# Kernel optimization log

Hardware: AMD Instinct MI355X
Metric: run time of the kernel (lower is better)

Reference implementation:

```python
import jax, jax.numpy as jnp
import numpy as np

NUM_HEADS = 8

def setup_inputs() -> dict:
    key = jax.random.key(0)
    k1, k2, k3 = jax.random.split(key, 3)
    query = jax.random.normal(k1, (2, 2048, 512), jnp.float32)   # [B, Tq, out_DIM]
    value = jax.random.normal(k2, (2, 2048, 64), jnp.float32)    # [B, Tv, out_DIM//H]
    conv_w = jax.random.normal(k3, (512, 64, 1), jnp.float32) * 0.05  # Conv1d weight [out, in, 1]
    conv_b = jnp.zeros((512,), jnp.float32)
    return {"query": query, "value": value, "conv_w": conv_w, "conv_b": conv_b}

def reference(query, value, conv_w, conv_b):
    B, Tq, D = query.shape
    H = NUM_HEADS
    dh = D // H  # 64
    # Conv1d with kernel_size=1 over the feature axis == pointwise linear
    k = jnp.einsum('btd,od->bto', value, conv_w[:, :, 0]) + conv_b  # [B, Tv, D]
    Tv = k.shape[1]
    # split heads
    qs = query.reshape(B, Tq, H, dh).transpose(0, 2, 1, 3)  # [B,H,Tq,dh]
    ks = k.reshape(B, Tv, H, dh).transpose(0, 2, 1, 3)      # [B,H,Tv,dh]
    vs = jnp.broadcast_to(value[:, None], (B, H, Tv, dh))   # v repeated per head
    # scaled dot product (normalize=True)
    qk = jnp.einsum('bhqd,bhkd->bhqk', qs, ks) * (dh ** -0.5)  # [B,H,Tq,Tv]
    # F.softmax(qk) with no dim on a 4D tensor uses legacy implicit dim=1 (heads)
    weights = jax.nn.softmax(qk, axis=1)
    ctx = jnp.einsum('bhqk,bhkd->bhqd', weights, vs)  # [B,H,Tq,dh]
    # combine heads
    return ctx.transpose(0, 2, 1, 3).reshape(B, Tq, H * dh)  # [B,Tq,D]
```

## Files before the change

kernel.cpp:

```cpp
#include <hip/hip_runtime.h>
#include <hip/hip_bf16.h>

#define BATCH 2
#define TSEQ  2048
#define DMODEL 512
#define NHEAD 8
#define DHEAD 64

typedef __bf16 bf16x2 __attribute__((ext_vector_type(2)));
typedef __bf16 bf16x4 __attribute__((ext_vector_type(4)));
typedef __bf16 bf16x8 __attribute__((ext_vector_type(8)));
typedef float  f32x4  __attribute__((ext_vector_type(4)));

#if __has_builtin(__builtin_amdgcn_exp2f)
#define EXP2(x) __builtin_amdgcn_exp2f(x)
#else
#define EXP2(x) exp2f(x)
#endif

__device__ __forceinline__ bf16x8 load_b8(const void* p) {
  return __builtin_bit_cast(bf16x8, *reinterpret_cast<const uint4*>(p));
}

__device__ __forceinline__ bf16x8 cvt8(const float* p) {
  float4 a = *reinterpret_cast<const float4*>(p);
  float4 b = *reinterpret_cast<const float4*>(p + 4);
  bf16x8 r;
  r[0] = (__bf16)a.x; r[1] = (__bf16)a.y; r[2] = (__bf16)a.z; r[3] = (__bf16)a.w;
  r[4] = (__bf16)b.x; r[5] = (__bf16)b.y; r[6] = (__bf16)b.z; r[7] = (__bf16)b.w;
  return r;
}

__device__ __forceinline__ bf16x8 cvt8s(const float* p, float s) {
  float4 a = *reinterpret_cast<const float4*>(p);
  float4 b = *reinterpret_cast<const float4*>(p + 4);
  bf16x8 r;
  r[0] = (__bf16)(a.x * s); r[1] = (__bf16)(a.y * s);
  r[2] = (__bf16)(a.z * s); r[3] = (__bf16)(a.w * s);
  r[4] = (__bf16)(b.x * s); r[5] = (__bf16)(b.y * s);
  r[6] = (__bf16)(b.z * s); r[7] = (__bf16)(b.w * s);
  return r;
}

__device__ __forceinline__ uint packbf(float a, float b) {
  uint ua = __builtin_bit_cast(uint, a);
  uint ub = __builtin_bit_cast(uint, b);
  return (ua >> 16) | (ub & 0xFFFF0000u);
}

#define KT_B   1048576
#define KT_T   8192
#define VT_B   131072
#define VT_K   2048

__global__ __launch_bounds__(256) void conv_kernel(
    const float* __restrict__ V,
    const float* __restrict__ W,
    const float* __restrict__ bias,
    __hip_bfloat16* __restrict__ Kt) {
  const int bx = blockIdx.x;
  const int b    = bx >> 7;
  const int tset = bx & 127;
  const int t0   = tset << 4;
  const int w  = threadIdx.x >> 6;
  const int l  = threadIdx.x & 63;
  const int lm = l & 15;
  const int lg = l >> 4;

  const float* vrow = V + ((size_t)(b * TSEQ + t0 + lm)) * DHEAD;
  bf16x8 av0 = cvt8(vrow + lg * 8);
  bf16x8 av1 = cvt8(vrow + 32 + lg * 8);

  #pragma unroll
  for (int n = 0; n < 8; ++n) {
    const int o0 = (w * 8 + n) * 16;
    const float* wrow = W + ((size_t)(o0 + lm)) * DHEAD;
    bf16x8 b0 = cvt8(wrow + lg * 8);
    bf16x8 b1 = cvt8(wrow + 32 + lg * 8);
    f32x4 acc = {0.f, 0.f, 0.f, 0.f};
    acc = __builtin_amdgcn_mfma_f32_16x16x32_bf16(av0, b0, acc, 0, 0, 0);
    acc = __builtin_amdgcn_mfma_f32_16x16x32_bf16(av1, b1, acc, 0, 0, 0);
    const int o   = o0 + lm;
    const int h   = o >> 6;
    const int gg  = (o >> 5) & 1;
    const int lgt = (o >> 3) & 3;
    const int j   = o & 7;
    const float bv = bias[o];
    const size_t kbase = (size_t)b * KT_B + (size_t)tset * KT_T +
                         h * 1024 + gg * 512 + lgt * 128 + j;
    #pragma unroll
    for (int r = 0; r < 4; ++r)
      Kt[kbase + (size_t)(lg * 4 + r) * 8] = __float2bfloat16(acc[r] + bv);
  }
}

__global__ __launch_bounds__(256) void vt_kernel(const float* __restrict__ V,
                                                 __hip_bfloat16* __restrict__ Vtile) {
  const int bx = blockIdx.x;
  const int b  = bx >> 5;
  const int t0 = (bx & 31) << 6;
  const int tid = threadIdx.x;
  __shared__ float tile[64][65];

  #pragma unroll
  for (int p = 0; p < 4; ++p) {
    const int r = p * 16 + (tid >> 4);
    const int c = (tid & 15) * 4;
    float4 v = *reinterpret_cast<const float4*>(
        &V[((size_t)(b * TSEQ + t0 + r)) * DHEAD + c]);
    tile[r][c]     = v.x;
    tile[r][c + 1] = v.y;
    tile[r][c + 2] = v.z;
    tile[r][c + 3] = v.w;
  }
  __syncthreads();

  const int dt = tid >> 6;
  const int l  = tid & 63;
  const int lm = l & 15;
  const int lg = l >> 4;
  #pragma unroll
  for (int ks2 = 0; ks2 < 2; ++ks2) {
    bf16x8 o;
    #pragma unroll
    for (int jj = 0; jj < 4; ++jj) {
      o[jj]     = (__bf16)tile[ks2 * 32 + lg * 4 + jj][dt * 16 + lm];
      o[jj + 4] = (__bf16)tile[ks2 * 32 + 16 + lg * 4 + jj][dt * 16 + lm];
    }
    *reinterpret_cast<uint4*>(
        Vtile + (size_t)b * VT_B + (size_t)((t0 >> 5) + ks2) * VT_K +
        dt * 512 + l * 8) = __builtin_bit_cast(uint4, o);
  }
}

template <int KCH>
__global__ __launch_bounds__(256, 2) void attn_kernel(
    const float* __restrict__ Q,
    const __hip_bfloat16* __restrict__ Kt,
    const __hip_bfloat16* __restrict__ Vtile,
    float* __restrict__ Out,
    float* __restrict__ P) {
  const int bx = blockIdx.x;
  int b, q0, c;
  if (KCH == 2) {
    const int L = (bx & 7) * 64 + (bx >> 3);
    b = L >> 8; const int rest = L & 255; q0 = (rest >> 1) << 4; c = rest & 1;
  } else {
    const int L = (bx & 7) * 32 + (bx >> 3);
    b = L >> 7; q0 = (L & 127) << 4; c = 0;
  }
  const int tid = threadIdx.x;
  const int w  = tid >> 6;
  const int l  = tid & 63;
  const int lm = l & 15;
  const int lg = l >> 4;

  constexpr int NRND = KCH == 2 ? 8 : 16;
  const int tsbase = c * 64;
  const int kvbase = c * 32;

  __shared__ __bf16 Qs[16 * 512];
  __shared__ __bf16 Ws[4][NHEAD][512];
  __shared__ float  Obuf[64][17];

  const float cl2 = 0.125f * 1.44269504f;
  {
    const int row = tid >> 4;
    const int seg = tid & 15;
    const float* src = Q + ((size_t)(b * TSEQ + q0 + row)) * DMODEL + seg * 32;
    char* base = (char*)Qs;
    const int sw = (row & 7) << 4;
    #pragma unroll
    for (int u = 0; u < 4; ++u) {
      bf16x8 v = cvt8s(src + u * 8, cl2);
      *(bf16x8*)(base + ((row * 1024 + seg * 64 + u * 16) ^ sw)) = v;
    }
  }
  __syncthreads();

  f32x4 accO[NHEAD];
  #pragma unroll
  for (int h = 0; h < NHEAD; ++h) accO[h] = (f32x4){0.f, 0.f, 0.f, 0.f};

  const char* qb = (const char*)Qs;
  const int qsw = (lm & 7) << 4;

  bf16x8 vA[4], vB[4];

  #define S_HALF(TSET, S2)                                                    \
    {                                                                         \
      const __hip_bfloat16* kb_ =                                             \
          Kt + (size_t)b * KT_B + (size_t)(TSET) * KT_T + l * 8;              \
      bf16x8 kf0[NHEAD], kf1[NHEAD];                                          \
      _Pragma("unroll")                                                       \
      for (int h = 0; h < NHEAD; ++h) {                                       \
        kf0[h] = load_b8(kb_ + h * 1024);                                     \
        kf1[h] = load_b8(kb_ + h * 1024 + 512);                               \
      }                                                                       \
      f32x4 sv[NHEAD];                                                        \
      __builtin_amdgcn_s_setprio(1);                                          \
      _Pragma("unroll")                                                       \
      for (int h = 0; h < NHEAD; ++h) {                                       \
        bf16x8 q0_ = *(const bf16x8*)(qb + ((lm * 1024 + h * 128 + lg * 16) ^ qsw)); \
        bf16x8 q1_ = *(const bf16x8*)(qb + ((lm * 1024 + h * 128 + 64 + lg * 16) ^ qsw)); \
        f32x4 t = {0.f, 0.f, 0.f, 0.f};                                       \
        t = __builtin_amdgcn_mfma_f32_16x16x32_bf16(kf0[h], q0_, t, 0, 0, 0); \
        t = __builtin_amdgcn_mfma_f32_16x16x32_bf16(kf1[h], q1_, t, 0, 0, 0); \
        sv[h] = t;                                                            \
      }                                                                       \
      __builtin_amdgcn_s_setprio(0);                                          \
      _Pragma("unroll")                                                       \
      for (int rp = 0; rp < 2; ++rp) {                                        \
        float w0_[NHEAD], w1_[NHEAD];                                         \
        float s0_ = 0.f, s1_ = 0.f;                                           \
        _Pragma("unroll")                                                     \
        for (int h = 0; h < NHEAD; ++h) { w0_[h] = EXP2(sv[h][2 * rp]);     s0_ += w0_[h]; } \
        _Pragma("unroll")                                                     \
        for (int h = 0; h < NHEAD; ++h) { w1_[h] = EXP2(sv[h][2 * rp + 1]); s1_ += w1_[h]; } \
        const float i0_ = __builtin_amdgcn_rcpf(s0_);                         \
        const float i1_ = __builtin_amdgcn_rcpf(s1_);                         \
        _Pragma("unroll")                                                     \
        for (int h = 0; h < NHEAD; ++h)                                       \
          wfu[h][(S2) * 2 + rp] = packbf(w0_[h] * i0_, w1_[h] * i1_);         \
      }                                                                       \
    }

  #define ROUND(R, VCUR, VNXT)                                                \
    {                                                                         \
      uint wfu[NHEAD][4];                                                     \
      const int ts0 = tsbase + (R) * 8 + w * 2;                               \
      S_HALF(ts0, 0);                                                         \
      S_HALF(ts0 + 1, 1);                                                     \
      _Pragma("unroll")                                                       \
      for (int h = 0; h < NHEAD; ++h)                                         \
        *reinterpret_cast<uint4*>((char*)(&Ws[w][h][0]) + l * 16) =           \
            uint4{wfu[h][0], wfu[h][1], wfu[h][2], wfu[h][3]};                \
      {                                                                       \
        const int RN = (R) < NRND - 1 ? (R) + 1 : NRND - 1;                   \
        const __hip_bfloat16* vb_ = Vtile + (size_t)b * VT_B +                \
            (size_t)(kvbase + RN * 4) * VT_K + w * 512 + l * 8;               \
        _Pragma("unroll")                                                     \
        for (int s = 0; s < 4; ++s) VNXT[s] = load_b8(vb_ + s * 2048);        \
      }                                                                       \
      __syncthreads();                                                        \
      __builtin_amdgcn_s_setprio(1);                                          \
      _Pragma("unroll")                                                       \
      for (int s = 0; s < 4; ++s) {                                           \
        _Pragma("unroll")                                                     \
        for (int h = 0; h < NHEAD; ++h) {                                     \
          bf16x8 wsf = *(const bf16x8*)((const char*)(&Ws[s][h][0]) + l * 16);\
          accO[h] = __builtin_amdgcn_mfma_f32_16x16x32_bf16(VCUR[s], wsf, accO[h], 0, 0, 0); \
        }                                                                     \
      }                                                                       \
      __builtin_amdgcn_s_setprio(0);                                          \
      __syncthreads();                                                        \
    }

  {
    const __hip_bfloat16* vb_ = Vtile + (size_t)b * VT_B +
        (size_t)kvbase * VT_K + w * 512 + l * 8;
    #pragma unroll
    for (int s = 0; s < 4; ++s) vA[s] = load_b8(vb_ + s * 2048);
  }

  #pragma unroll 1
  for (int rp2 = 0; rp2 < NRND / 2; ++rp2) {
    ROUND(2 * rp2,     vA, vB);
    ROUND(2 * rp2 + 1, vB, vA);
  }

  #undef ROUND
  #undef S_HALF

  float* outbase = (KCH == 2)
      ? P + ((size_t)((b * 128 + (q0 >> 4)) * 2 + c)) * 8192
      : Out + ((size_t)(b * TSEQ + q0)) * DMODEL;
  #pragma unroll
  for (int h = 0; h < NHEAD; ++h) {
    #pragma unroll
    for (int r = 0; r < 4; ++r)
      Obuf[w * 16 + lg * 4 + r][lm] = accO[h][r];
    __syncthreads();
    {
      const int q  = tid >> 4;
      const int d0 = (tid & 15) * 4;
      float4 s = {Obuf[d0][q], Obuf[d0 + 1][q], Obuf[d0 + 2][q], Obuf[d0 + 3][q]};
      *reinterpret_cast<float4*>(&outbase[(size_t)q * 512 + h * DHEAD + d0]) = s;
    }
    __syncthreads();
  }
}

__global__ void reduce_kernel(const float4* __restrict__ P,
                              float4* __restrict__ Out) {
  const int g = blockIdx.x * 256 + threadIdx.x;
  const int f = g << 2;
  const int d = f & 511;
  const int q = (f >> 9) & 2047;
  const int b = f >> 20;
  const size_t p0 = (((size_t)(b * 128 + (q >> 4)) * 2) * 8192 +
                     (size_t)(q & 15) * 512 + d) >> 2;
  float4 a = P[p0];
  float4 c = P[p0 + 2048];
  Out[g] = float4{a.x + c.x, a.y + c.y, a.z + c.z, a.w + c.w};
}

extern "C" void kernel_launch(void* const* d_in, const int* in_sizes, int n_in,
                              void* d_out, int out_size, void* d_ws, size_t ws_size,
                              hipStream_t stream) {
  const float* Q    = (const float*)d_in[0];
  const float* V    = (const float*)d_in[1];
  const float* W    = (const float*)d_in[2];
  const float* bias = (const float*)d_in[3];
  float* Out = (float*)d_out;

  __hip_bfloat16* Ktb = (__hip_bfloat16*)d_ws;
  __hip_bfloat16* Vtb = Ktb + (size_t)BATCH * KT_B;
  const size_t pOff = 4u * 1024 * 1024 + 512u * 1024;
  float* P = (float*)((char*)d_ws + pOff);
  const bool split = ws_size >= pOff + (size_t)512 * 8192 * 4;

  conv_kernel<<<256, 256, 0, stream>>>(V, W, bias, Ktb);
  vt_kernel<<<64, 256, 0, stream>>>(V, Vtb);
  if (split) {
    attn_kernel<2><<<512, 256, 0, stream>>>(Q, Ktb, Vtb, Out, P);
    reduce_kernel<<<2048, 256, 0, stream>>>((const float4*)P, (float4*)Out);
  } else {
    attn_kernel<1><<<256, 256, 0, stream>>>(Q, Ktb, Vtb, Out, P);
  }
}
```

Measured before the change: 53.88 us.

## Replace split-KV attention plus reduce with single 512-thread block per query tile

Drops the two-chunk KV split and its separate reduction kernel, launching 256 blocks of 512 threads (8 waves) that each cover the full key range for a 16-query tile. Each wave computes scores for 2 key tiles per round, and in the PV step each wave handles 4 heads by one 16-column d-slice. The Q shared-memory layout is changed to a per-head linear layout without swizzle, and V prefetch double-buffering is replaced by a per-round load of 8 fragments. This removes the partial-sum write, the reduce launch and its memory traffic. In exchange it uses fewer, larger blocks with one block per CU, and it loses the V prefetch overlap.

After: 71.98 us. 33.6% more time.

```diff
diff --git a/kernel.cpp b/kernel.cpp
--- a/kernel.cpp
+++ b/kernel.cpp
@@ -133,79 +133,64 @@
   }
 }
 
-template <int KCH>
-__global__ __launch_bounds__(256, 2) void attn_kernel(
+__global__ __launch_bounds__(512, 1) void attn_kernel(
     const float* __restrict__ Q,
     const __hip_bfloat16* __restrict__ Kt,
     const __hip_bfloat16* __restrict__ Vtile,
-    float* __restrict__ Out,
-    float* __restrict__ P) {
+    float* __restrict__ Out) {
   const int bx = blockIdx.x;
-  int b, q0, c;
-  if (KCH == 2) {
-    const int L = (bx & 7) * 64 + (bx >> 3);
-    b = L >> 8; const int rest = L & 255; q0 = (rest >> 1) << 4; c = rest & 1;
-  } else {
-    const int L = (bx & 7) * 32 + (bx >> 3);
-    b = L >> 7; q0 = (L & 127) << 4; c = 0;
-  }
+  const int L  = (bx & 7) * 32 + (bx >> 3);
+  const int b  = L >> 7;
+  const int q0 = (L & 127) << 4;
   const int tid = threadIdx.x;
-  const int w  = tid >> 6;
-  const int l  = tid & 63;
-  const int lm = l & 15;
-  const int lg = l >> 4;
-
-  constexpr int NRND = KCH == 2 ? 8 : 16;
-  const int tsbase = c * 64;
-  const int kvbase = c * 32;
-
-  __shared__ __bf16 Qs[16 * 512];
-  __shared__ __bf16 Ws[4][NHEAD][512];
-  __shared__ float  Obuf[64][17];
+  const int w   = tid >> 6;
+  const int l   = tid & 63;
+  const int lm  = l & 15;
+  const int lg  = l >> 4;
+  const int myh0 = (w >> 2) * 4;
+  const int mydt = w & 3;
+
+  __shared__ __bf16 Qs[8192];
+  __shared__ __bf16 Ws[8][NHEAD][512];
+  __shared__ float  Obuf[2][64][17];
 
   const float cl2 = 0.125f * 1.44269504f;
   {
-    const int row = tid >> 4;
-    const int seg = tid & 15;
-    const float* src = Q + ((size_t)(b * TSEQ + q0 + row)) * DMODEL + seg * 32;
-    char* base = (char*)Qs;
-    const int sw = (row & 7) << 4;
-    #pragma unroll
-    for (int u = 0; u < 4; ++u) {
-      bf16x8 v = cvt8s(src + u * 8, cl2);
-      *(bf16x8*)(base + ((row * 1024 + seg * 64 + u * 16) ^ sw)) = v;
+    const int hg = tid >> 5;
+    const int wi = tid & 31;
+    const int h = hg >> 1, g = hg & 1;
+    #pragma unroll
+    for (int u = 0; u < 2; ++u) {
+      const int ll  = u * 32 + wi;
+      const int row = ll & 15;
+      const int seg = ll >> 4;
+      const float* src = Q + ((size_t)(b * TSEQ + q0 + row)) * DMODEL +
+                         h * DHEAD + g * 32 + seg * 8;
+      bf16x8 v = cvt8s(src, cl2);
+      *(bf16x8*)((char*)Qs + hg * 1024 + ll * 16) = v;
     }
   }
   __syncthreads();
 
-  f32x4 accO[NHEAD];
-  #pragma unroll
-  for (int h = 0; h < NHEAD; ++h) accO[h] = (f32x4){0.f, 0.f, 0.f, 0.f};
-
-  const char* qb = (const char*)Qs;
-  const int qsw = (lm & 7) << 4;
-
-  bf16x8 vA[4], vB[4];
+  f32x4 accO[4];
+  #pragma unroll
+  for (int hh = 0; hh < 4; ++hh) accO[hh] = (f32x4){0.f, 0.f, 0.f, 0.f};
 
   #define S_HALF(TSET, S2)                                                    \
     {                                                                         \
       const __hip_bfloat16* kb_ =                                             \
           Kt + (size_t)b * KT_B + (size_t)(TSET) * KT_T + l * 8;              \
-      bf16x8 kf0[NHEAD], kf1[NHEAD];                                          \
-      _Pragma("unroll")                                                       \
-      for (int h = 0; h < NHEAD; ++h) {                                       \
-        kf0[h] = load_b8(kb_ + h * 1024);                                     \
-        kf1[h] = load_b8(kb_ + h * 1024 + 512);                               \
-      }                                                                       \
       f32x4 sv[NHEAD];                                                        \
       __builtin_amdgcn_s_setprio(1);                                          \
       _Pragma("unroll")                                                       \
       for (int h = 0; h < NHEAD; ++h) {                                       \
-        bf16x8 q0_ = *(const bf16x8*)(qb + ((lm * 1024 + h * 128 + lg * 16) ^ qsw)); \
-        bf16x8 q1_ = *(const bf16x8*)(qb + ((lm * 1024 + h * 128 + 64 + lg * 16) ^ qsw)); \
+        bf16x8 kf0 = load_b8(kb_ + h * 1024);                                 \
+        bf16x8 kf1 = load_b8(kb_ + h * 1024 + 512);                           \
+        bf16x8 q0_ = *(const bf16x8*)((const char*)Qs + (h * 2) * 1024 + l * 16);     \
+        bf16x8 q1_ = *(const bf16x8*)((const char*)Qs + (h * 2 + 1) * 1024 + l * 16); \
         f32x4 t = {0.f, 0.f, 0.f, 0.f};                                       \
-        t = __builtin_amdgcn_mfma_f32_16x16x32_bf16(kf0[h], q0_, t, 0, 0, 0); \
-        t = __builtin_amdgcn_mfma_f32_16x16x32_bf16(kf1[h], q1_, t, 0, 0, 0); \
+        t = __builtin_amdgcn_mfma_f32_16x16x32_bf16(kf0, q0_, t, 0, 0, 0);    \
+        t = __builtin_amdgcn_mfma_f32_16x16x32_bf16(kf1, q1_, t, 0, 0, 0);    \
         sv[h] = t;                                                            \
       }                                                                       \
       __builtin_amdgcn_s_setprio(0);                                          \
@@ -225,84 +210,60 @@
       }                                                                       \
     }
 
-  #define ROUND(R, VCUR, VNXT)                                                \
-    {                                                                         \
-      uint wfu[NHEAD][4];                                                     \
-      const int ts0 = tsbase + (R) * 8 + w * 2;                               \
-      S_HALF(ts0, 0);                                                         \
-      S_HALF(ts0 + 1, 1);                                                     \
-      _Pragma("unroll")                                                       \
-      for (int h = 0; h < NHEAD; ++h)                                         \
-        *reinterpret_cast<uint4*>((char*)(&Ws[w][h][0]) + l * 16) =           \
-            uint4{wfu[h][0], wfu[h][1], wfu[h][2], wfu[h][3]};                \
-      {                                                                       \
-        const int RN = (R) < NRND - 1 ? (R) + 1 : NRND - 1;                   \
-        const __hip_bfloat16* vb_ = Vtile + (size_t)b * VT_B +                \
-            (size_t)(kvbase + RN * 4) * VT_K + w * 512 + l * 8;               \
-        _Pragma("unroll")                                                     \
-        for (int s = 0; s < 4; ++s) VNXT[s] = load_b8(vb_ + s * 2048);        \
-      }                                                                       \
-      __syncthreads();                                                        \
-      __builtin_amdgcn_s_setprio(1);                                          \
-      _Pragma("unroll")                                                       \
-      for (int s = 0; s < 4; ++s) {                                           \
-        _Pragma("unroll")                                                     \
-        for (int h = 0; h < NHEAD; ++h) {                                     \
-          bf16x8 wsf = *(const bf16x8*)((const char*)(&Ws[s][h][0]) + l * 16);\
-          accO[h] = __builtin_amdgcn_mfma_f32_16x16x32_bf16(VCUR[s], wsf, accO[h], 0, 0, 0); \
-        }                                                                     \
-      }                                                                       \
-      __builtin_amdgcn_s_setprio(0);                                          \
-      __syncthreads();                                                        \
-    }
-
-  {
-    const __hip_bfloat16* vb_ = Vtile + (size_t)b * VT_B +
-        (size_t)kvbase * VT_K + w * 512 + l * 8;
-    #pragma unroll
-    for (int s = 0; s < 4; ++s) vA[s] = load_b8(vb_ + s * 2048);
-  }
-
   #pragma unroll 1
-  for (int rp2 = 0; rp2 < NRND / 2; ++rp2) {
-    ROUND(2 * rp2,     vA, vB);
-    ROUND(2 * rp2 + 1, vB, vA);
-  }
-
-  #undef ROUND
+  for (int R = 0; R < 8; ++R) {
+    bf16x8 vc[8];
+    {
+      const __hip_bfloat16* vb_ = Vtile + (size_t)b * VT_B +
+          (size_t)(R * 8) * VT_K + mydt * 512 + l * 8;
+      #pragma unroll
+      for (int s = 0; s < 8; ++s) vc[s] = load_b8(vb_ + s * VT_K);
+    }
+
+    uint wfu[NHEAD][4];
+    const int ts0 = R * 16 + w * 2;
+    S_HALF(ts0, 0);
+    S_HALF(ts0 + 1, 1);
+    #pragma unroll
+    for (int h = 0; h < NHEAD; ++h)
+      *reinterpret_cast<uint4*>((char*)(&Ws[w][h][0]) + l * 16) =
+          uint4{wfu[h][0], wfu[h][1], wfu[h][2], wfu[h][3]};
+    __syncthreads();
+
+    __builtin_amdgcn_s_setprio(1);
+    #pragma unroll
+    for (int s = 0; s < 8; ++s) {
+      #pragma unroll
+      for (int hh = 0; hh < 4; ++hh) {
+        bf16x8 wsf = *(const bf16x8*)((const char*)(&Ws[s][myh0 + hh][0]) + l * 16);
+        accO[hh] = __builtin_amdgcn_mfma_f32_16x16x32_bf16(vc[s], wsf, accO[hh], 0, 0, 0);
+      }
+    }
+    __builtin_amdgcn_s_setprio(0);
+    __syncthreads();
+  }
+
   #undef S_HALF
 
-  float* outbase = (KCH == 2)
-      ? P + ((size_t)((b * 128 + (q0 >> 4)) * 2 + c)) * 8192
-      : Out + ((size_t)(b * TSEQ + q0)) * DMODEL;
-  #pragma unroll
-  for (int h = 0; h < NHEAD; ++h) {
+  float* obase = Out + ((size_t)(b * TSEQ + q0)) * DMODEL;
+  #pragma unroll
+  for (int hh = 0; hh < 4; ++hh) {
     #pragma unroll
     for (int r = 0; r < 4; ++r)
-      Obuf[w * 16 + lg * 4 + r][lm] = accO[h][r];
+      Obuf[w >> 2][mydt * 16 + lg * 4 + r][lm] = accO[hh][r];
     __syncthreads();
     {
-      const int q  = tid >> 4;
-      const int d0 = (tid & 15) * 4;
-      float4 s = {Obuf[d0][q], Obuf[d0 + 1][q], Obuf[d0 + 2][q], Obuf[d0 + 3][q]};
-      *reinterpret_cast<float4*>(&outbase[(size_t)q * 512 + h * DHEAD + d0]) = s;
-    }
-    __syncthreads();
-  }
-}
-
-__global__ void reduce_kernel(const float4* __restrict__ P,
-                              float4* __restrict__ Out) {
-  const int g = blockIdx.x * 256 + threadIdx.x;
-  const int f = g << 2;
-  const int d = f & 511;
-  const int q = (f >> 9) & 2047;
-  const int b = f >> 20;
-  const size_t p0 = (((size_t)(b * 128 + (q >> 4)) * 2) * 8192 +
-                     (size_t)(q & 15) * 512 + d) >> 2;
-  float4 a = P[p0];
-  float4 c = P[p0 + 2048];
-  Out[g] = float4{a.x + c.x, a.y + c.y, a.z + c.z, a.w + c.w};
+      const int gg = tid >> 8;
+      const int wi = tid & 255;
+      const int q  = wi >> 4;
+      const int d0 = (wi & 15) * 4;
+      const int h  = gg * 4 + hh;
+      float4 s = {Obuf[gg][d0][q], Obuf[gg][d0 + 1][q],
+                  Obuf[gg][d0 + 2][q], Obuf[gg][d0 + 3][q]};
+      *reinterpret_cast<float4*>(&obase[(size_t)q * DMODEL + h * DHEAD + d0]) = s;
+    }
+    __syncthreads();
+  }
 }
 
 extern "C" void kernel_launch(void* const* d_in, const int* in_sizes, int n_in,
@@ -316,16 +277,8 @@
 
   __hip_bfloat16* Ktb = (__hip_bfloat16*)d_ws;
   __hip_bfloat16* Vtb = Ktb + (size_t)BATCH * KT_B;
-  const size_t pOff = 4u * 1024 * 1024 + 512u * 1024;
-  float* P = (float*)((char*)d_ws + pOff);
-  const bool split = ws_size >= pOff + (size_t)512 * 8192 * 4;
 
   conv_kernel<<<256, 256, 0, stream>>>(V, W, bias, Ktb);
   vt_kernel<<<64, 256, 0, stream>>>(V, Vtb);
-  if (split) {
-    attn_kernel<2><<<512, 256, 0, stream>>>(Q, Ktb, Vtb, Out, P);
-    reduce_kernel<<<2048, 256, 0, stream>>>((const float4*)P, (float4*)Out);
-  } else {
-    attn_kernel<1><<<256, 256, 0, stream>>>(Q, Ktb, Vtb, Out, P);
-  }
-}
+  attn_kernel<<<BATCH * (TSEQ / 16), 512, 0, stream>>>(Q, Ktb, Vtb, Out);
+}
```
